# Performance work log

Measured on AMD Instinct MI355X. Metric: run time of the kernel, lower is better.

## Reference

```python
import jax, jax.numpy as jnp
import numpy as np

B, L, D = 128, 256, 1024


def setup_inputs() -> dict:
    key = jax.random.key(0)
    k = jax.random.split(key, 6)
    return {
        "tok0": jax.random.normal(k[0], (B, L, D), jnp.float32),
        "tok1": jax.random.normal(k[1], (B, L, D), jnp.float32),
        "glob0": jax.random.normal(k[2], (B, D), jnp.float32),
        "glob1": jax.random.normal(k[3], (B, D), jnp.float32),
        "len0": jax.random.randint(k[4], (B,), 0, L),
        "len1": jax.random.randint(k[5], (B,), 0, L),
    }


def _side_sums(tok, glob, lens):
    """JSD expectations for one view.

    Equivalent to the original ragged concat + dense mask construction:
    non-positive entries of get_positive_expectation contribute
    -softplus(0) + log2 = 0, and positive entries of
    get_negative_expectation contribute softplus(0) + 0 - log2 = 0,
    so only the masked terms below survive. Padding tokens (l >= lens[b])
    never exist in the original concatenated matrix, so they are excluded.
    """
    b, l_max = tok.shape[0], tok.shape[1]
    # scores: token x sentence-global, [B, L, B]
    res = jnp.einsum("bld,gd->blg", tok, glob)
    valid = jnp.arange(l_max)[None, :] < lens[:, None]          # [B, L]
    same = jnp.eye(b, dtype=bool)[:, None, :]                    # [B, 1, B]
    pos = valid[:, :, None] & same                               # token vs own sentence
    neg = valid[:, :, None] & ~same                              # token vs other sentences
    e_pos = jnp.sum(jnp.where(pos, -jax.nn.softplus(-res), 0.0))
    e_neg = jnp.sum(jnp.where(neg, jax.nn.softplus(-res) + res, 0.0))
    return e_pos, e_neg


def reference(tok0, tok1, glob0, glob1, len0, len1):
    len0 = jnp.clip(len0, 1, None)
    len1 = jnp.clip(len1, 1, None)
    avg_sentence_length = (jnp.mean(len0.astype(jnp.float32))
                           + jnp.mean(len1.astype(jnp.float32))) / 2.0

    ep0, en0 = _side_sums(tok0, glob0, len0)
    ep1, en1 = _side_sums(tok1, glob1, len1)

    num_nodes = (jnp.sum(len0) + jnp.sum(len1)).astype(jnp.float32)
    num_graphs = jnp.float32(B)
    e_pos = (ep0 + ep1) / num_nodes
    e_neg = (en0 + en1) / (num_nodes * (num_graphs - 1.0))
    loss = e_neg - e_pos
    return loss, avg_sentence_length
```

## Files before the change

kernel.cpp:

```cpp
#include <hip/hip_runtime.h>
#include <hip/hip_bf16.h>

#define B_SENT 128
#define L_TOK  256
#define D_DIM  1024
#define TM     64

typedef __attribute__((ext_vector_type(8))) short bf16x8;
typedef __attribute__((ext_vector_type(4))) float f32x4;

__device__ __forceinline__ unsigned short f2bf(float f) {
    return __builtin_bit_cast(unsigned short, __float2bfloat16(f));
}
__device__ __forceinline__ float softplus_f(float x) {
    float ax = fabsf(x);
    return fmaxf(x, 0.0f) + __logf(1.0f + __expf(-ax));
}
__device__ __forceinline__ bf16x8 cvt8(const float4& lo, const float4& hi) {
    bf16x8 u;
    u[0] = (short)f2bf(lo.x); u[1] = (short)f2bf(lo.y);
    u[2] = (short)f2bf(lo.z); u[3] = (short)f2bf(lo.w);
    u[4] = (short)f2bf(hi.x); u[5] = (short)f2bf(hi.y);
    u[6] = (short)f2bf(hi.z); u[7] = (short)f2bf(hi.w);
    return u;
}

__global__ __launch_bounds__(256) void pack_g_kernel(
    const float* __restrict__ g0, const float* __restrict__ g1,
    short* __restrict__ packed)
{
    const int idx  = blockIdx.x * 256 + threadIdx.x;
    const int lane = idx & 63;
    const int n    = (idx >> 6) & 7;
    const int ks   = (idx >> 9) & 1;
    const int kb   = (idx >> 10) & 15;
    const int side = idx >> 14;
    const int row  = n * 16 + (lane & 15);
    const int col  = kb * 64 + ks * 32 + (lane >> 4) * 8;
    const float* g = side ? g1 : g0;
    const float4 v0 = *reinterpret_cast<const float4*>(&g[(size_t)row * D_DIM + col]);
    const float4 v1 = *reinterpret_cast<const float4*>(&g[(size_t)row * D_DIM + col + 4]);
    *reinterpret_cast<bf16x8*>(&packed[(size_t)idx * 8]) = cvt8(v0, v1);
}

__global__ __launch_bounds__(256, 4) void mi_main_kernel(
    const float* __restrict__ tok0, const float* __restrict__ tok1,
    const int* __restrict__ len0, const int* __restrict__ len1,
    const short* __restrict__ packed, float* __restrict__ acc_ws)
{
    const int side = blockIdx.y;
    const float* tok = side ? tok1 : tok0;
    const int*   len = side ? len1 : len0;

    const int tile   = blockIdx.x;
    const int tb     = tile * TM;
    const int b_sent = tile >> 2;
    const int vstart = (tile & 3) * TM;
    const int count  = max(1, len[b_sent]) - vstart;
    if (count <= 0) return;

    const int tid  = threadIdx.x;
    const int wave = tid >> 6;
    const int lane = tid & 63;
    const int lrow = lane & 15;
    const int kgrp = lane >> 4;

    __shared__ short Bs[2][8192];
    __shared__ float sred[8];

    const short* bsrc = packed + (size_t)(side * 16) * 8192;
    const int  arow   = wave * 16 + lrow;
    const bool avalid = arow < count;
    const float* aptr = tok + (size_t)(tb + arow) * D_DIM + kgrp * 8;

    f32x4 acc[8];
#pragma unroll
    for (int n = 0; n < 8; ++n) acc[n] = (f32x4){0.f, 0.f, 0.f, 0.f};

    const float4 z4 = (float4){0.f, 0.f, 0.f, 0.f};
    float4 Ac0 = z4, Ac1 = z4, Ac2 = z4, Ac3 = z4;

    {
        const short* bp = bsrc + tid * 8;
#pragma unroll
        for (int i = 0; i < 4; ++i)
            *reinterpret_cast<bf16x8*>(&Bs[0][i * 2048 + tid * 8]) =
                *reinterpret_cast<const bf16x8*>(bp + i * 2048);
        if (avalid) {
            Ac0 = *reinterpret_cast<const float4*>(aptr);
            Ac1 = *reinterpret_cast<const float4*>(aptr + 4);
            Ac2 = *reinterpret_cast<const float4*>(aptr + 32);
            Ac3 = *reinterpret_cast<const float4*>(aptr + 36);
        }
    }
    __syncthreads();

    auto compute = [&](int buf, const bf16x8& af0, const bf16x8& af1) {
#pragma unroll
        for (int n = 0; n < 8; ++n) {
            bf16x8 b = *reinterpret_cast<const bf16x8*>(&Bs[buf][(n * 64 + lane) * 8]);
            acc[n] = __builtin_amdgcn_mfma_f32_16x16x32_bf16(af0, b, acc[n], 0, 0, 0);
        }
#pragma unroll
        for (int n = 0; n < 8; ++n) {
            bf16x8 b = *reinterpret_cast<const bf16x8*>(&Bs[buf][((8 + n) * 64 + lane) * 8]);
            acc[n] = __builtin_amdgcn_mfma_f32_16x16x32_bf16(af1, b, acc[n], 0, 0, 0);
        }
    };

#pragma unroll 1
    for (int kb = 0; kb < 15; ++kb) {
        const int cur = kb & 1, nxt = cur ^ 1;

        const short* bp = bsrc + (size_t)(kb + 1) * 8192 + tid * 8;
        bf16x8 s0 = *reinterpret_cast<const bf16x8*>(bp);
        bf16x8 s1 = *reinterpret_cast<const bf16x8*>(bp + 2048);
        bf16x8 s2 = *reinterpret_cast<const bf16x8*>(bp + 4096);
        bf16x8 s3 = *reinterpret_cast<const bf16x8*>(bp + 6144);
        float4 An0 = z4, An1 = z4, An2 = z4, An3 = z4;
        {
            const float* ap = aptr + (kb + 1) * 64;
            if (avalid) {
                An0 = *reinterpret_cast<const float4*>(ap);
                An1 = *reinterpret_cast<const float4*>(ap + 4);
                An2 = *reinterpret_cast<const float4*>(ap + 32);
                An3 = *reinterpret_cast<const float4*>(ap + 36);
            }
        }
        __builtin_amdgcn_sched_barrier(0);

        const bf16x8 af0 = cvt8(Ac0, Ac1);
        const bf16x8 af1 = cvt8(Ac2, Ac3);
        compute(cur, af0, af1);

        *reinterpret_cast<bf16x8*>(&Bs[nxt][tid * 8])        = s0;
        *reinterpret_cast<bf16x8*>(&Bs[nxt][2048 + tid * 8]) = s1;
        *reinterpret_cast<bf16x8*>(&Bs[nxt][4096 + tid * 8]) = s2;
        *reinterpret_cast<bf16x8*>(&Bs[nxt][6144 + tid * 8]) = s3;

        Ac0 = An0; Ac1 = An1; Ac2 = An2; Ac3 = An3;
        __syncthreads();
    }
    {
        const bf16x8 af0 = cvt8(Ac0, Ac1);
        const bf16x8 af1 = cvt8(Ac2, Ac3);
        compute(1, af0, af1);
    }

    float ep = 0.f, en = 0.f;
#pragma unroll
    for (int n = 0; n < 8; ++n) {
        const int g = n * 16 + lrow;
#pragma unroll
        for (int j = 0; j < 4; ++j) {
            const int rl = wave * 16 + kgrp * 4 + j;
            if (rl < count) {
                float res = acc[n][j];
                float sp  = softplus_f(res);
                if (g == b_sent) ep += res - sp;
                else             en += sp;
            }
        }
    }

#pragma unroll
    for (int off = 32; off; off >>= 1) {
        ep += __shfl_down(ep, off);
        en += __shfl_down(en, off);
    }
    if (lane == 0) { sred[wave * 2] = ep; sred[wave * 2 + 1] = en; }
    __syncthreads();
    if (tid == 0) {
        float tep = sred[0] + sred[2] + sred[4] + sred[6];
        float ten = sred[1] + sred[3] + sred[5] + sred[7];
        atomicAdd(&acc_ws[side * 2 + 0], tep);
        atomicAdd(&acc_ws[side * 2 + 1], ten);
    }
}

__global__ void mi_finalize_kernel(const int* __restrict__ len0,
                                   const int* __restrict__ len1,
                                   const float* __restrict__ acc_ws,
                                   float* __restrict__ out)
{
    const int lane = threadIdx.x;
    int s0 = 0, s1 = 0;
    for (int i = lane; i < B_SENT; i += 64) {
        s0 += max(1, len0[i]);
        s1 += max(1, len1[i]);
    }
#pragma unroll
    for (int off = 32; off; off >>= 1) {
        s0 += __shfl_down(s0, off);
        s1 += __shfl_down(s1, off);
    }
    if (lane == 0) {
        const float num_nodes = (float)(s0 + s1);
        const float ep = acc_ws[0] + acc_ws[2];
        const float en = acc_ws[1] + acc_ws[3];
        out[0] = en / (num_nodes * (float)(B_SENT - 1)) - ep / num_nodes;
        out[1] = ((float)s0 + (float)s1) / (2.0f * (float)B_SENT);
    }
}

extern "C" void kernel_launch(void* const* d_in, const int* in_sizes, int n_in,
                              void* d_out, int out_size, void* d_ws, size_t ws_size,
                              hipStream_t stream) {
    const float* tok0  = (const float*)d_in[0];
    const float* tok1  = (const float*)d_in[1];
    const float* glob0 = (const float*)d_in[2];
    const float* glob1 = (const float*)d_in[3];
    const int*   len0  = (const int*)d_in[4];
    const int*   len1  = (const int*)d_in[5];
    float* out = (float*)d_out;

    float* acc    = (float*)d_ws;
    short* packed = (short*)((char*)d_ws + 256);

    hipMemsetAsync(d_ws, 0, 256, stream);
    pack_g_kernel<<<128, 256, 0, stream>>>(glob0, glob1, packed);

    dim3 grid(32768 / TM, 2);
    mi_main_kernel<<<grid, 256, 0, stream>>>(tok0, tok1, len0, len1, packed, acc);
    mi_finalize_kernel<<<1, 64, 0, stream>>>(len0, len1, acc, out);
}
```

Baseline: 58.66 us.

## Stage A and B tiles via direct global-to-LDS loads with BK=32

Replaces register-staged global loads of the fp32 token tile and the packed bf16 global tile with direct global_load_lds transfers into double-buffered LDS. The K block shrinks from 64 to 32, and the glob packing layout changes to match. The aim is to cut register pressure and the extra LDS write traffic while keeping loads in flight behind the MFMA work. The cost is twice as many loop iterations and barriers. A rows past the sentence length are now loaded unmasked, which is wasted bandwidth, though the epilogue still excludes them.

```diff
diff --git a/kernel.cpp b/kernel.cpp
--- a/kernel.cpp
+++ b/kernel.cpp
@@ -5,6 +5,8 @@
 #define L_TOK  256
 #define D_DIM  1024
 #define TM     64
+#define BK     32
+#define NKB    (D_DIM / BK)
 
 typedef __attribute__((ext_vector_type(8))) short bf16x8;
 typedef __attribute__((ext_vector_type(4))) float f32x4;
@@ -16,13 +18,19 @@
     float ax = fabsf(x);
     return fmaxf(x, 0.0f) + __logf(1.0f + __expf(-ax));
 }
-__device__ __forceinline__ bf16x8 cvt8(const float4& lo, const float4& hi) {
+__device__ __forceinline__ bf16x8 cvt8f(const float4& lo, const float4& hi) {
     bf16x8 u;
     u[0] = (short)f2bf(lo.x); u[1] = (short)f2bf(lo.y);
     u[2] = (short)f2bf(lo.z); u[3] = (short)f2bf(lo.w);
     u[4] = (short)f2bf(hi.x); u[5] = (short)f2bf(hi.y);
     u[6] = (short)f2bf(hi.z); u[7] = (short)f2bf(hi.w);
     return u;
+}
+
+__device__ __forceinline__ void gl_lds16(const void* g, void* l) {
+    __builtin_amdgcn_global_load_lds(
+        (const __attribute__((address_space(1))) unsigned int*)g,
+        (__attribute__((address_space(3))) unsigned int*)l, 16, 0, 0);
 }
 
 __global__ __launch_bounds__(256) void pack_g_kernel(
@@ -32,15 +40,14 @@
     const int idx  = blockIdx.x * 256 + threadIdx.x;
     const int lane = idx & 63;
     const int n    = (idx >> 6) & 7;
-    const int ks   = (idx >> 9) & 1;
-    const int kb   = (idx >> 10) & 15;
+    const int kb   = (idx >> 9) & 31;
     const int side = idx >> 14;
     const int row  = n * 16 + (lane & 15);
-    const int col  = kb * 64 + ks * 32 + (lane >> 4) * 8;
+    const int col  = kb * 32 + (lane >> 4) * 8;
     const float* g = side ? g1 : g0;
     const float4 v0 = *reinterpret_cast<const float4*>(&g[(size_t)row * D_DIM + col]);
     const float4 v1 = *reinterpret_cast<const float4*>(&g[(size_t)row * D_DIM + col + 4]);
-    *reinterpret_cast<bf16x8*>(&packed[(size_t)idx * 8]) = cvt8(v0, v1);
+    *reinterpret_cast<bf16x8*>(&packed[(size_t)idx * 8]) = cvt8f(v0, v1);
 }
 
 __global__ __launch_bounds__(256, 4) void mi_main_kernel(
@@ -55,8 +62,7 @@
     const int tile   = blockIdx.x;
     const int tb     = tile * TM;
     const int b_sent = tile >> 2;
-    const int vstart = (tile & 3) * TM;
-    const int count  = max(1, len[b_sent]) - vstart;
+    const int count  = max(1, len[b_sent]) - (tile & 3) * TM;
     if (count <= 0) return;
 
     const int tid  = threadIdx.x;
@@ -65,86 +71,53 @@
     const int lrow = lane & 15;
     const int kgrp = lane >> 4;
 
-    __shared__ short Bs[2][8192];
+    __shared__ float As[2][2048];
+    __shared__ short Bs[2][4096];
     __shared__ float sred[8];
 
-    const short* bsrc = packed + (size_t)(side * 16) * 8192;
-    const int  arow   = wave * 16 + lrow;
-    const bool avalid = arow < count;
-    const float* aptr = tok + (size_t)(tb + arow) * D_DIM + kgrp * 8;
+    const float* asrc = tok + (size_t)(tb + wave * 16 + lrow) * D_DIM + kgrp * 8;
+    const short* bchunk = packed + (size_t)side * NKB * 4096;
+    const int br0 = ((wave * 2 + 0) * 64 + lane) * 8;
+    const int br1 = ((wave * 2 + 1) * 64 + lane) * 8;
 
     f32x4 acc[8];
 #pragma unroll
     for (int n = 0; n < 8; ++n) acc[n] = (f32x4){0.f, 0.f, 0.f, 0.f};
 
-    const float4 z4 = (float4){0.f, 0.f, 0.f, 0.f};
-    float4 Ac0 = z4, Ac1 = z4, Ac2 = z4, Ac3 = z4;
+    auto stage = [&](int buf, int kb) {
+        const float* a = asrc + kb * BK;
+        gl_lds16(a,     &As[buf][(wave * 2 + 0) * 256]);
+        gl_lds16(a + 4, &As[buf][(wave * 2 + 1) * 256]);
+        const short* bc = bchunk + (size_t)kb * 4096;
+        gl_lds16(bc + br0, &Bs[buf][(wave * 2 + 0) * 512]);
+        gl_lds16(bc + br1, &Bs[buf][(wave * 2 + 1) * 512]);
+    };
 
-    {
-        const short* bp = bsrc + tid * 8;
-#pragma unroll
-        for (int i = 0; i < 4; ++i)
-            *reinterpret_cast<bf16x8*>(&Bs[0][i * 2048 + tid * 8]) =
-                *reinterpret_cast<const bf16x8*>(bp + i * 2048);
-        if (avalid) {
-            Ac0 = *reinterpret_cast<const float4*>(aptr);
-            Ac1 = *reinterpret_cast<const float4*>(aptr + 4);
-            Ac2 = *reinterpret_cast<const float4*>(aptr + 32);
-            Ac3 = *reinterpret_cast<const float4*>(aptr + 36);
-        }
-    }
-    __syncthreads();
-
-    auto compute = [&](int buf, const bf16x8& af0, const bf16x8& af1) {
+    auto compute = [&](int buf) {
+        const f32x4 alo = *reinterpret_cast<const f32x4*>(
+            &As[buf][(wave * 2 + 0) * 256 + lane * 4]);
+        const f32x4 ahi = *reinterpret_cast<const f32x4*>(
+            &As[buf][(wave * 2 + 1) * 256 + lane * 4]);
+        bf16x8 af;
+        af[0] = (short)f2bf(alo[0]); af[1] = (short)f2bf(alo[1]);
+        af[2] = (short)f2bf(alo[2]); af[3] = (short)f2bf(alo[3]);
+        af[4] = (short)f2bf(ahi[0]); af[5] = (short)f2bf(ahi[1]);
+        af[6] = (short)f2bf(ahi[2]); af[7] = (short)f2bf(ahi[3]);
 #pragma unroll
         for (int n = 0; n < 8; ++n) {
             bf16x8 b = *reinterpret_cast<const bf16x8*>(&Bs[buf][(n * 64 + lane) * 8]);
-            acc[n] = __builtin_amdgcn_mfma_f32_16x16x32_bf16(af0, b, acc[n], 0, 0, 0);
-        }
-#pragma unroll
-        for (int n = 0; n < 8; ++n) {
-            bf16x8 b = *reinterpret_cast<const bf16x8*>(&Bs[buf][((8 + n) * 64 + lane) * 8]);
-            acc[n] = __builtin_amdgcn_mfma_f32_16x16x32_bf16(af1, b, acc[n], 0, 0, 0);
+            acc[n] = __builtin_amdgcn_mfma_f32_16x16x32_bf16(af, b, acc[n], 0, 0, 0);
         }
     };
 
+    stage(0, 0);
+    __syncthreads();
 #pragma unroll 1
-    for (int kb = 0; kb < 15; ++kb) {
-        const int cur = kb & 1, nxt = cur ^ 1;
-
-        const short* bp = bsrc + (size_t)(kb + 1) * 8192 + tid * 8;
-        bf16x8 s0 = *reinterpret_cast<const bf16x8*>(bp);
-        bf16x8 s1 = *reinterpret_cast<const bf16x8*>(bp + 2048);
-        bf16x8 s2 = *reinterpret_cast<const bf16x8*>(bp + 4096);
-        bf16x8 s3 = *reinterpret_cast<const bf16x8*>(bp + 6144);
-        float4 An0 = z4, An1 = z4, An2 = z4, An3 = z4;
-        {
-            const float* ap = aptr + (kb + 1) * 64;
-            if (avalid) {
-                An0 = *reinterpret_cast<const float4*>(ap);
-                An1 = *reinterpret_cast<const float4*>(ap + 4);
-                An2 = *reinterpret_cast<const float4*>(ap + 32);
-                An3 = *reinterpret_cast<const float4*>(ap + 36);
-            }
-        }
-        __builtin_amdgcn_sched_barrier(0);
-
-        const bf16x8 af0 = cvt8(Ac0, Ac1);
-        const bf16x8 af1 = cvt8(Ac2, Ac3);
-        compute(cur, af0, af1);
-
-        *reinterpret_cast<bf16x8*>(&Bs[nxt][tid * 8])        = s0;
-        *reinterpret_cast<bf16x8*>(&Bs[nxt][2048 + tid * 8]) = s1;
-        *reinterpret_cast<bf16x8*>(&Bs[nxt][4096 + tid * 8]) = s2;
-        *reinterpret_cast<bf16x8*>(&Bs[nxt][6144 + tid * 8]) = s3;
-
-        Ac0 = An0; Ac1 = An1; Ac2 = An2; Ac3 = An3;
+    for (int kb = 0; kb < NKB; ++kb) {
+        const int cur = kb & 1;
+        if (kb + 1 < NKB) stage(cur ^ 1, kb + 1);
+        compute(cur);
         __syncthreads();
-    }
-    {
-        const bf16x8 af0 = cvt8(Ac0, Ac1);
-        const bf16x8 af1 = cvt8(Ac2, Ac3);
-        compute(1, af0, af1);
     }
 
     float ep = 0.f, en = 0.f;
```

Result: slower. 62.76 us (+7.0%).
